# Kernel optimization log

Measured on AMD Instinct MI355X. Metric: run time of the kernel, lower is better.

Reference implementation:

```python
import jax, jax.numpy as jnp
import numpy as np

D_MODEL = 1024
D_HIDDEN = 2048
BATCH = 2
SEQ = 4096


def setup_inputs() -> dict:
    key = jax.random.key(0)
    ks = jax.random.split(key, 14)
    d, h = D_MODEL, D_HIDDEN
    s_d = 1.0 / np.sqrt(d)
    s_h = 1.0 / np.sqrt(h)
    x = jax.random.normal(ks[0], (BATCH, SEQ, d), jnp.float32)
    W1 = jax.random.normal(ks[1], (d, d), jnp.float32) * s_d
    W2 = jax.random.normal(ks[2], (d, d), jnp.float32) * s_d
    Wlast = jax.random.normal(ks[3], (d, d), jnp.float32) * s_d
    conv_w = jax.random.normal(ks[4], (d, 1, 3), jnp.float32) * 0.5  # depthwise (O, I/g=1, K)
    conv_b = jnp.zeros((d,), jnp.float32)
    A = jax.random.normal(ks[5], (h,), jnp.float32)
    Wb = jax.random.normal(ks[6], (h, d), jnp.float32) * s_d
    bb = jnp.zeros((h,), jnp.float32)
    Wc = jax.random.normal(ks[7], (d, h), jnp.float32) * s_h
    bc = jnp.zeros((d,), jnp.float32)
    Wd = jax.random.normal(ks[8], (d, d), jnp.float32) * s_d
    bd = jnp.zeros((d,), jnp.float32)
    # small delta so cumsum(delta*A) over SEQ steps stays O(1) (avoids exp overflow)
    Wdelta = jax.random.normal(ks[9], (h, d), jnp.float32) * 0.01
    bdelta = jnp.full((h,), -8.0, jnp.float32)
    return dict(x=x, W1=W1, conv_w=conv_w, conv_b=conv_b, A=A, Wb=Wb, bb=bb,
                Wc=Wc, bc=bc, Wd=Wd, bd=bd, Wdelta=Wdelta, bdelta=bdelta,
                W2=W2, Wlast=Wlast)


def reference(x, W1, conv_w, conv_b, A, Wb, bb, Wc, bc, Wd, bd, Wdelta, bdelta, W2, Wlast):
    # x: [B, L, d]
    x1 = x @ W1.T  # linear1 (no bias)
    # depthwise conv1d, kernel 3, pad 1, groups = d_model
    xc = jax.lax.conv_general_dilated(
        x1.transpose(0, 2, 1), conv_w,
        window_strides=(1,), padding=[(1, 1)],
        feature_group_count=D_MODEL,
        dimension_numbers=('NCH', 'OIH', 'NCH')) + conv_b[None, :, None]
    xa = jax.nn.silu(xc.transpose(0, 2, 1))  # [B, L, d]
    # SSM: delta/A/B discretization + cumprod-cumsum scan along sequence
    delta = jax.nn.softplus(xa @ Wdelta.T + bdelta)  # [B, L, h]
    A_bar = jnp.exp(delta * A)
    B_bar = delta * (xa @ Wb.T + bb)
    A_cum = jnp.cumprod(A_bar, axis=1)
    h_st = jnp.cumsum(B_bar / A_cum, axis=1) * A_cum  # [B, L, h]
    out_ssm = (h_st @ Wc.T + bc) + (xa @ Wd.T + bd)  # [B, L, d]
    # gated residual
    x_res = jax.nn.silu(out_ssm @ W2.T)
    z = out_ssm * x_res
    return out_ssm + z @ Wlast.T
```

## Files before the change

kernel.cpp:

```cpp
#include <hip/hip_runtime.h>
#include <cstdint>
#include <cstddef>

#define DMODEL 1024
#define DH 2048
#define BATCH 2
#define SEQ 4096
#define MROWS (BATCH*SEQ)
#define CHUNK 64
#define NCHUNK (SEQ/CHUNK)

typedef unsigned short u16;
typedef __attribute__((ext_vector_type(8))) short bf16x8;
typedef __attribute__((ext_vector_type(4))) float f32x4;

__device__ __forceinline__ u16 f2bf(float f) {
    union { float f; unsigned u; } v; v.f = f;
    unsigned r = v.u + 0x7FFFu + ((v.u >> 16) & 1u);
    return (u16)(r >> 16);
}
__device__ __forceinline__ float bf2f(u16 h) {
    union { unsigned u; float f; } v; v.u = ((unsigned)h) << 16; return v.f;
}

__device__ __forceinline__ float softplus_fast(float x) {
    if (x < -4.f) return __expf(x);
    return (x > 0.f) ? (x + log1pf(__expf(-x))) : log1pf(__expf(x));
}
__device__ __forceinline__ float silu_fast(float v) {
    return v * __fdividef(1.f, 1.f + __expf(-v));
}

__global__ void cvt_bf16(const float* __restrict__ src, u16* __restrict__ dst, int n4) {
    int i = blockIdx.x * blockDim.x + threadIdx.x;
    if (i >= n4) return;
    const float4 v = reinterpret_cast<const float4*>(src)[i];
    ushort4 o;
    o.x = f2bf(v.x); o.y = f2bf(v.y); o.z = f2bf(v.z); o.w = f2bf(v.w);
    reinterpret_cast<ushort4*>(dst)[i] = o;
}

__device__ __forceinline__ void gload_lds16(const void* g, void* l) {
    __builtin_amdgcn_global_load_lds(
        (const __attribute__((address_space(1))) void*)g,
        (__attribute__((address_space(3))) void*)l,
        16, 0, 0);
}

template<int EP, bool TWOK>
__global__ __launch_bounds__(256, 4) void gemm_bt(
    const u16* __restrict__ A1, const u16* __restrict__ B1, int K1,
    const u16* __restrict__ A2, const u16* __restrict__ B2, int K2,
    float* __restrict__ C, u16* __restrict__ Cb, u16* __restrict__ Cb2,
    const float* __restrict__ bias, const float* __restrict__ bias2,
    const float* __restrict__ aux,
    int M, int N)
{
    __shared__ __align__(16) char smem[32768];
    u16* As = (u16*)smem;
    u16* Bs = (u16*)(smem + 16384);
    float* ep = (float*)smem;

    const int tid = threadIdx.x;

    const int nwg = gridDim.x * gridDim.y;
    int wg = blockIdx.y * gridDim.x + blockIdx.x;
    wg = (wg & 7) * (nwg >> 3) + (wg >> 3);
    const int stile = wg >> 6;
    const int t64   = wg & 63;
    const int nSn   = gridDim.x >> 3;
    const int sm = (nSn > 0) ? stile / nSn : stile;
    const int sn = (nSn > 0) ? stile - sm * nSn : 0;
    const int m0 = (sm * 8 + (t64 >> 3)) * 128;
    const int n0 = (sn * 8 + (t64 & 7)) * 128;

    const int wave = tid >> 6, lane = tid & 63;
    const int wr = (wave >> 1) * 64;
    const int wc = (wave & 1) * 64;
    const int fr = lane & 15, fq = lane >> 4;

    f32x4 acc[4][4];
    #pragma unroll
    for (int m = 0; m < 4; m++)
        #pragma unroll
        for (int n = 0; n < 4; n++) acc[m][n] = f32x4{0.f, 0.f, 0.f, 0.f};

    const int nt1 = K1 >> 6;
    const int nt  = TWOK ? nt1 + (K2 >> 6) : nt1;

    for (int t = 0; t < nt; ++t) {
        const u16* A = A1; const u16* B = B1; int K = K1; int k0 = t << 6;
        if (TWOK && t >= nt1) { A = A2; B = B2; K = K2; k0 = (t - nt1) << 6; }
        #pragma unroll
        for (int i = 0; i < 4; ++i) {
            const int g = i*256 + tid;
            const int r = g >> 3;
            const int ch = (g & 7) ^ (r & 7);
            gload_lds16(A + (size_t)(m0 + r)*K + (k0 + ch*8), (char*)As + (size_t)g*16);
            gload_lds16(B + (size_t)(n0 + r)*K + (k0 + ch*8), (char*)Bs + (size_t)g*16);
        }
        __syncthreads();

        #pragma unroll
        for (int kk = 0; kk < 2; ++kk) {
            bf16x8 af[4], bfr[4];
            #pragma unroll
            for (int m = 0; m < 4; m++) {
                const int r = wr + m*16 + fr;
                af[m] = *reinterpret_cast<const bf16x8*>(
                    (const char*)As + r*128 + (((kk*4 + fq) ^ (r & 7)) * 16));
            }
            #pragma unroll
            for (int n = 0; n < 4; n++) {
                const int r = wc + n*16 + fr;
                bfr[n] = *reinterpret_cast<const bf16x8*>(
                    (const char*)Bs + r*128 + (((kk*4 + fq) ^ (r & 7)) * 16));
            }
            #pragma unroll
            for (int m = 0; m < 4; m++)
                #pragma unroll
                for (int n = 0; n < 4; n++)
                    acc[m][n] = __builtin_amdgcn_mfma_f32_16x16x32_bf16(af[m], bfr[n], acc[m][n], 0, 0, 0);
        }
        __syncthreads();
    }

    const bool isDelta = (EP == 4) ? (n0 < DH) : false;
    #pragma unroll
    for (int c = 0; c < 4; ++c) {
        if ((wave >> 1) == (c >> 1)) {
            const int mb = (c & 1) * 2;
            #pragma unroll
            for (int mi = 0; mi < 2; mi++) {
                #pragma unroll
                for (int n = 0; n < 4; n++) {
                    const int col = wc + n*16 + fr;
                    #pragma unroll
                    for (int j = 0; j < 4; j++)
                        ep[(mi*16 + fq*4 + j)*132 + col] = acc[mb + mi][n][j];
                }
            }
        }
        __syncthreads();
        #pragma unroll
        for (int p = 0; p < 4; ++p) {
            const int idx = p*256 + tid;
            const int row = idx >> 5, c4 = idx & 31;
            float4 v = *reinterpret_cast<const float4*>(&ep[row*132 + c4*4]);
            const int rg   = m0 + c*32 + row;
            const int colg = n0 + c4*4;
            if constexpr (EP == 4) {
                const int cc = isDelta ? colg : (colg - DH);
                const float4 bv = *reinterpret_cast<const float4*>(
                    (isDelta ? bias : bias2) + cc);
                ushort4 o;
                if (isDelta) {
                    o.x = f2bf(softplus_fast(v.x + bv.x));
                    o.y = f2bf(softplus_fast(v.y + bv.y));
                    o.z = f2bf(softplus_fast(v.z + bv.z));
                    o.w = f2bf(softplus_fast(v.w + bv.w));
                } else {
                    o.x = f2bf(v.x + bv.x); o.y = f2bf(v.y + bv.y);
                    o.z = f2bf(v.z + bv.z); o.w = f2bf(v.w + bv.w);
                }
                *reinterpret_cast<ushort4*>((isDelta ? Cb : Cb2) + (size_t)rg*DH + cc) = o;
            } else {
                if (bias) {
                    const float4 b1 = *reinterpret_cast<const float4*>(bias + colg);
                    v.x += b1.x; v.y += b1.y; v.z += b1.z; v.w += b1.w;
                }
                if (bias2) {
                    const float4 b2 = *reinterpret_cast<const float4*>(bias2 + colg);
                    v.x += b2.x; v.y += b2.y; v.z += b2.z; v.w += b2.w;
                }
                const size_t gidx = (size_t)rg * N + colg;
                if constexpr (EP == 0) {
                    ushort4 o = { f2bf(v.x), f2bf(v.y), f2bf(v.z), f2bf(v.w) };
                    *reinterpret_cast<ushort4*>(Cb + gidx) = o;
                } else if constexpr (EP == 1) {
                    *reinterpret_cast<float4*>(C + gidx) = v;
                    ushort4 o = { f2bf(v.x), f2bf(v.y), f2bf(v.z), f2bf(v.w) };
                    *reinterpret_cast<ushort4*>(Cb + gidx) = o;
                } else if constexpr (EP == 2) {
                    const float4 a = *reinterpret_cast<const float4*>(aux + gidx);
                    ushort4 o = { f2bf(a.x * silu_fast(v.x)), f2bf(a.y * silu_fast(v.y)),
                                  f2bf(a.z * silu_fast(v.z)), f2bf(a.w * silu_fast(v.w)) };
                    *reinterpret_cast<ushort4*>(Cb + gidx) = o;
                } else {
                    const float4 a = *reinterpret_cast<const float4*>(aux + gidx);
                    float4 o = { a.x + v.x, a.y + v.y, a.z + v.z, a.w + v.w };
                    *reinterpret_cast<float4*>(C + gidx) = o;
                }
            }
        }
        __syncthreads();
    }
}

__global__ void conv_silu8(const u16* __restrict__ x1, const float* __restrict__ cw,
                           const float* __restrict__ cb, u16* __restrict__ xab) {
    int t = blockIdx.x * blockDim.x + threadIdx.x;
    int c8  = t & (DMODEL/8 - 1);
    int row = t >> 7;
    int l = row & (SEQ - 1);
    const int c0 = c8 * 8;
    const size_t i0 = (size_t)row * DMODEL + c0;
    bf16x8 v0 = *reinterpret_cast<const bf16x8*>(x1 + i0);
    bf16x8 vm = {}; if (l > 0)       vm = *reinterpret_cast<const bf16x8*>(x1 + i0 - DMODEL);
    bf16x8 vp = {}; if (l < SEQ - 1) vp = *reinterpret_cast<const bf16x8*>(x1 + i0 + DMODEL);
    if (l == 0)       vm = bf16x8{};
    if (l == SEQ - 1) vp = bf16x8{};
    bf16x8 o;
    #pragma unroll
    for (int j = 0; j < 8; ++j) {
        const int c = c0 + j;
        float v = cw[c*3+0]*bf2f((u16)vm[j]) + cw[c*3+1]*bf2f((u16)v0[j])
                + cw[c*3+2]*bf2f((u16)vp[j]) + cb[c];
        o[j] = (short)f2bf(silu_fast(v));
    }
    *reinterpret_cast<bf16x8*>(xab + i0) = o;
}

__global__ void scan_chunks(const u16* __restrict__ delta, const u16* __restrict__ pBv,
                            const float* __restrict__ Avec,
                            float* __restrict__ cA, float* __restrict__ cB) {
    const int c = blockIdx.x * blockDim.x + threadIdx.x;
    const int q = blockIdx.y;
    const int b = blockIdx.z;
    const float Ac = Avec[c];
    float hA = 1.f, hB = 0.f;
    size_t base = ((size_t)b*SEQ + q*CHUNK)*DH + c;
    for (int j = 0; j < CHUNK; ++j) {
        float d = bf2f(delta[base]);
        float Abar = __expf(d * Ac);
        hA *= Abar;
        hB = Abar*hB + d * bf2f(pBv[base]);
        base += DH;
    }
    size_t o = ((size_t)b*NCHUNK + q)*DH + c;
    cA[o] = hA; cB[o] = hB;
}

__global__ void scan_prefix(const float* __restrict__ cA, const float* __restrict__ cB,
                            float* __restrict__ cH) {
    const int t = blockIdx.x * blockDim.x + threadIdx.x;
    const int b = t >> 11;
    const int c = t & (DH - 1);
    float h = 0.f;
    size_t o = ((size_t)b*NCHUNK)*DH + c;
    float a = cA[o], bb = cB[o];
    for (int q = 0; q < NCHUNK; ++q) {
        const size_t on = o + DH;
        float a2 = 0.f, b2 = 0.f;
        if (q + 1 < NCHUNK) { a2 = cA[on]; b2 = cB[on]; }
        cH[o] = h;
        h = a*h + bb;
        a = a2; bb = b2; o = on;
    }
}

__global__ void scan_apply(const u16* __restrict__ delta, const u16* __restrict__ pBv,
                           const float* __restrict__ Avec, const float* __restrict__ cH,
                           u16* __restrict__ hstb) {
    const int c = blockIdx.x * blockDim.x + threadIdx.x;
    const int q = blockIdx.y;
    const int b = blockIdx.z;
    const float Ac = Avec[c];
    float h = cH[((size_t)b*NCHUNK + q)*DH + c];
    size_t base = ((size_t)b*SEQ + q*CHUNK)*DH + c;
    for (int j = 0; j < CHUNK; ++j) {
        float d = bf2f(delta[base]);
        float Abar = __expf(d * Ac);
        h = Abar*h + d * bf2f(pBv[base]);
        hstb[base] = f2bf(h);
        base += DH;
    }
}

extern "C" void kernel_launch(void* const* d_in, const int* in_sizes, int n_in,
                              void* d_out, int out_size, void* d_ws, size_t ws_size,
                              hipStream_t stream) {
    const float* x      = (const float*)d_in[0];
    const float* W1     = (const float*)d_in[1];
    const float* conv_w = (const float*)d_in[2];
    const float* conv_b = (const float*)d_in[3];
    const float* Avec   = (const float*)d_in[4];
    const float* Wb     = (const float*)d_in[5];
    const float* bb     = (const float*)d_in[6];
    const float* Wc     = (const float*)d_in[7];
    const float* bc     = (const float*)d_in[8];
    const float* Wd     = (const float*)d_in[9];
    const float* bd     = (const float*)d_in[10];
    const float* Wdelta = (const float*)d_in[11];
    const float* bdelta = (const float*)d_in[12];
    const float* W2     = (const float*)d_in[13];
    const float* Wlast  = (const float*)d_in[14];
    float* out = (float*)d_out;
    (void)in_sizes; (void)n_in; (void)out_size;

    struct Ptrs {
        u16 *sW;
        float *cA, *cB, *cH;
        u16 *xb, *x1b, *xab, *delta, *pBv, *ossb, *hstb, *zb;
        float *oss;
        size_t total;
    };
    auto layout = [&](int passes) -> Ptrs {
        Ptrs P{};
        const size_t Mp = MROWS / passes;
        const int nb = BATCH / passes;
        size_t off = 0;
        auto al = [&](size_t bytes) -> char* {
            char* p = (char*)d_ws + off; off += (bytes + 255) & ~(size_t)255; return p;
        };
        P.sW  = (u16*)al((size_t)2*DH*DMODEL*2);
        P.cA  = (float*)al((size_t)nb*NCHUNK*DH*4);
        P.cB  = (float*)al((size_t)nb*NCHUNK*DH*4);
        P.cH  = (float*)al((size_t)nb*NCHUNK*DH*4);
        char* RA = al(Mp*DMODEL*2);
        char* RB = al(Mp*DMODEL*2);
        char* RC = al(Mp*DMODEL*2);
        char* RD = al(Mp*DH*2);
        char* RE = al(Mp*DH*2);
        char* RF = al(Mp*DH*2);
        P.xb    = (u16*)RA; P.ossb = (u16*)RA;
        P.x1b   = (u16*)RB; P.zb   = (u16*)RB;
        P.xab   = (u16*)RC;
        P.delta = (u16*)RD; P.oss  = (float*)RD;
        P.pBv   = (u16*)RE;
        P.hstb  = (u16*)RF;
        P.total = off;
        return P;
    };

    int passes = (ws_size >= layout(1).total) ? 1 : 2;
    Ptrs P = layout(passes);
    if (ws_size < P.total) return;
    const int Mp = MROWS / passes;
    const int nb = BATCH / passes;

    const dim3 blk(256);
    auto cvt = [&](const float* s, u16* d, size_t n) {
        int n4 = (int)(n / 4);
        cvt_bf16<<<dim3((n4 + 255)/256), blk, 0, stream>>>(s, d, n4);
    };
    const dim3 gD (DMODEL/128, Mp/128);
    const dim3 gDB(2*DH/128,   Mp/128);
    u16* sW2 = P.sW + (size_t)DH*DMODEL;

    for (int p = 0; p < passes; ++p) {
        const float* x_p  = x  + (size_t)p*Mp*DMODEL;
        float*      out_p = out + (size_t)p*Mp*DMODEL;

        cvt(x_p, P.xb, (size_t)Mp*DMODEL);
        cvt(W1, P.sW, (size_t)DMODEL*DMODEL);
        gemm_bt<0,false><<<gD, blk, 0, stream>>>(P.xb, P.sW, DMODEL, nullptr, nullptr, 0,
                                                 nullptr, P.x1b, nullptr, nullptr, nullptr, nullptr, Mp, DMODEL);
        conv_silu8<<<dim3(Mp*DMODEL/8/256), blk, 0, stream>>>(P.x1b, conv_w, conv_b, P.xab);
        cvt(Wdelta, P.sW, (size_t)DH*DMODEL);
        cvt(Wb,     sW2,  (size_t)DH*DMODEL);
        gemm_bt<4,false><<<gDB, blk, 0, stream>>>(P.xab, P.sW, DMODEL, nullptr, nullptr, 0,
                                                  nullptr, P.delta, P.pBv, bdelta, bb, nullptr, Mp, 2*DH);
        scan_chunks<<<dim3(DH/256, NCHUNK, nb), blk, 0, stream>>>(P.delta, P.pBv, Avec, P.cA, P.cB);
        scan_prefix<<<dim3(nb*DH/256), blk, 0, stream>>>(P.cA, P.cB, P.cH);
        scan_apply <<<dim3(DH/256, NCHUNK, nb), blk, 0, stream>>>(P.delta, P.pBv, Avec, P.cH, P.hstb);
        cvt(Wd, P.sW, (size_t)DMODEL*DMODEL);
        cvt(Wc, sW2,  (size_t)DMODEL*DH);
        gemm_bt<1,true><<<gD, blk, 0, stream>>>(P.xab, P.sW, DMODEL, P.hstb, sW2, DH,
                                                P.oss, P.ossb, nullptr, bd, bc, nullptr, Mp, DMODEL);
        cvt(W2, P.sW, (size_t)DMODEL*DMODEL);
        gemm_bt<2,false><<<gD, blk, 0, stream>>>(P.ossb, P.sW, DMODEL, nullptr, nullptr, 0,
                                                 nullptr, P.zb, nullptr, nullptr, nullptr, P.oss, Mp, DMODEL);
        cvt(Wlast, P.sW, (size_t)DMODEL*DMODEL);
        gemm_bt<3,false><<<gD, blk, 0, stream>>>(P.zb, P.sW, DMODEL, nullptr, nullptr, 0,
                                                 out_p, nullptr, nullptr, nullptr, nullptr, P.oss, Mp, DMODEL);
    }
}
```

Measured before the change: 307.2 us.

## Use 256x256-tile pipelined MFMA GEMM for delta/B projection

Adds a new GEMM kernel with 256x256 output tiles, 512 threads, a double-buffered 128KB LDS pipeline fed by direct global-to-LDS loads with XOR swizzling, and a workgroup remap that groups tiles per XCD. It is used for the fused Wdelta/Wb projection, the largest GEMM. Larger tiles raise arithmetic intensity and cut global traffic. The cost is low occupancy (one workgroup per CU) and higher register pressure from the 8x4 accumulator fragments.

```diff
diff --git a/kernel.cpp b/kernel.cpp
--- a/kernel.cpp
+++ b/kernel.cpp
@@ -45,6 +45,160 @@
         (const __attribute__((address_space(1))) void*)g,
         (__attribute__((address_space(3))) void*)l,
         16, 0, 0);
+}
+
+template<int EP>
+__global__ __launch_bounds__(512, 2) void gemm8p(
+    const u16* __restrict__ A, const u16* __restrict__ Bm, int K,
+    u16* __restrict__ Cb, u16* __restrict__ Cb2,
+    const float* __restrict__ bias, const float* __restrict__ bias2,
+    int M, int N)
+{
+    __shared__ __align__(16) char smem[131072];
+    const int tid = threadIdx.x;
+
+    const int nwg = gridDim.x * gridDim.y;
+    int wg = blockIdx.y * gridDim.x + blockIdx.x;
+    wg = (wg & 7) * (nwg >> 3) + (wg >> 3);
+    const int stile = wg >> 6;
+    const int t64   = wg & 63;
+    const int nSn   = gridDim.x >> 3;
+    const int sm = (nSn > 0) ? stile / nSn : stile;
+    const int sn = (nSn > 0) ? stile - sm * nSn : 0;
+    const int m0 = (sm * 8 + (t64 >> 3)) * 256;
+    const int n0 = (sn * 8 + (t64 & 7)) * 256;
+
+    const int wave = tid >> 6, lane = tid & 63;
+    const int gm16 = (wave >> 2) * 16;
+    const int gn   = wave & 3;
+    const int fr = lane & 15, fq = lane >> 4;
+    const int fx = fr & 7;
+
+    f32x4 acc[8][4];
+    #pragma unroll
+    for (int m = 0; m < 8; m++)
+        #pragma unroll
+        for (int n = 0; n < 4; n++) acc[m][n] = f32x4{0.f, 0.f, 0.f, 0.f};
+
+    const int nt = K >> 6;
+
+    auto stage_half = [&](int t, int isB, int h) {
+        const u16* src = isB ? Bm : A;
+        const int base0 = (isB ? n0 : m0) + h * 128;
+        char* dst = smem + (size_t)(((t & 1) * 65536) + isB * 32768 + h * 16384);
+        #pragma unroll
+        for (int j = 0; j < 2; ++j) {
+            const int g = j*512 + tid;
+            const int r = g >> 3;
+            const int ch = (g & 7) ^ (r & 7);
+            gload_lds16(src + (size_t)(base0 + r)*K + (t*64 + ch*8), dst + (size_t)g*16);
+        }
+    };
+
+    stage_half(0,1,0); stage_half(0,1,1); stage_half(0,0,0); stage_half(0,0,1);
+    stage_half(1,1,0); stage_half(1,1,1); stage_half(1,0,0);
+    asm volatile("s_waitcnt vmcnt(6)" ::: "memory");
+    __builtin_amdgcn_s_barrier();
+    __builtin_amdgcn_sched_barrier(0);
+
+    for (int t = 0; t < nt; ++t) {
+        const char* Abase = smem + (t & 1) * 65536;
+        const char* Bbase = Abase + 32768;
+        bf16x8 bfr[4][2];
+        #pragma unroll
+        for (int q = 0; q < 4; ++q) {
+            bf16x8 af[2][2];
+            #pragma unroll
+            for (int i = 0; i < 2; ++i) {
+                const int m = 2*q + i;
+                const int rl = (m & 3)*32 + gm16 + fr;
+                #pragma unroll
+                for (int kk = 0; kk < 2; ++kk)
+                    af[i][kk] = *reinterpret_cast<const bf16x8*>(
+                        Abase + (m >> 2)*16384 + rl*128 + (((kk*4 + fq) ^ fx) * 16));
+            }
+            if (q == 0) {
+                #pragma unroll
+                for (int n = 0; n < 4; ++n) {
+                    const int cl = (gn & 1)*64 + n*16 + fr;
+                    #pragma unroll
+                    for (int kk = 0; kk < 2; ++kk)
+                        bfr[n][kk] = *reinterpret_cast<const bf16x8*>(
+                            Bbase + (gn >> 1)*16384 + cl*128 + (((kk*4 + fq) ^ fx) * 16));
+                }
+            }
+            if (q == 0) { if (t + 1 < nt) stage_half(t + 1, 0, 1); }
+            else if (t + 2 < nt) {
+                if (q == 1)      stage_half(t + 2, 1, 0);
+                else if (q == 2) stage_half(t + 2, 1, 1);
+                else             stage_half(t + 2, 0, 0);
+            }
+            __builtin_amdgcn_s_barrier();
+            asm volatile("s_waitcnt lgkmcnt(0)" ::: "memory");
+            __builtin_amdgcn_sched_barrier(0);
+            __builtin_amdgcn_s_setprio(1);
+            #pragma unroll
+            for (int i = 0; i < 2; ++i)
+                #pragma unroll
+                for (int n = 0; n < 4; ++n)
+                    #pragma unroll
+                    for (int kk = 0; kk < 2; ++kk)
+                        acc[2*q + i][n] = __builtin_amdgcn_mfma_f32_16x16x32_bf16(
+                            af[i][kk], bfr[n][kk], acc[2*q + i][n], 0, 0, 0);
+            __builtin_amdgcn_s_setprio(0);
+            if (q == 3) {
+                if (t + 2 < nt) { asm volatile("s_waitcnt vmcnt(6)" ::: "memory"); }
+                else            { asm volatile("s_waitcnt vmcnt(0)" ::: "memory"); }
+            }
+            __builtin_amdgcn_s_barrier();
+            __builtin_amdgcn_sched_barrier(0);
+        }
+    }
+
+    float* ep = (float*)smem;
+    const bool isDelta = (EP == 4) ? (n0 < DH) : false;
+    #pragma unroll
+    for (int c = 0; c < 8; ++c) {
+        #pragma unroll
+        for (int n = 0; n < 4; ++n) {
+            const int col = gn*64 + n*16 + fr;
+            #pragma unroll
+            for (int j = 0; j < 4; ++j)
+                ep[(gm16 + fq*4 + j)*260 + col] = acc[c][n][j];
+        }
+        __syncthreads();
+        #pragma unroll
+        for (int p = 0; p < 4; ++p) {
+            const int idx = p*512 + tid;
+            const int row = idx >> 6, c4 = idx & 63;
+            float4 v = *reinterpret_cast<const float4*>(&ep[row*260 + c4*4]);
+            const int rg   = m0 + c*32 + row;
+            const int colg = n0 + c4*4;
+            if constexpr (EP == 4) {
+                const int cc = isDelta ? colg : (colg - DH);
+                const float4 bv = *reinterpret_cast<const float4*>(
+                    (isDelta ? bias : bias2) + cc);
+                ushort4 o;
+                if (isDelta) {
+                    o.x = f2bf(softplus_fast(v.x + bv.x));
+                    o.y = f2bf(softplus_fast(v.y + bv.y));
+                    o.z = f2bf(softplus_fast(v.z + bv.z));
+                    o.w = f2bf(softplus_fast(v.w + bv.w));
+                } else {
+                    o.x = f2bf(v.x + bv.x); o.y = f2bf(v.y + bv.y);
+                    o.z = f2bf(v.z + bv.z); o.w = f2bf(v.w + bv.w);
+                }
+                *reinterpret_cast<ushort4*>((isDelta ? Cb : Cb2) + (size_t)rg*DH + cc) = o;
+            } else {
+                float4 b1 = {0,0,0,0};
+                if (bias) b1 = *reinterpret_cast<const float4*>(bias + colg);
+                ushort4 o = { f2bf(v.x + b1.x), f2bf(v.y + b1.y),
+                              f2bf(v.z + b1.z), f2bf(v.w + b1.w) };
+                *reinterpret_cast<ushort4*>(Cb + (size_t)rg*N + colg) = o;
+            }
+        }
+        __syncthreads();
+    }
 }
 
 template<int EP, bool TWOK>
@@ -344,8 +498,8 @@
         int n4 = (int)(n / 4);
         cvt_bf16<<<dim3((n4 + 255)/256), blk, 0, stream>>>(s, d, n4);
     };
-    const dim3 gD (DMODEL/128, Mp/128);
-    const dim3 gDB(2*DH/128,   Mp/128);
+    const dim3 gD  (DMODEL/128, Mp/128);
+    const dim3 gDB8(2*DH/256,   Mp/256);
     u16* sW2 = P.sW + (size_t)DH*DMODEL;
 
     for (int p = 0; p < passes; ++p) {
@@ -359,8 +513,8 @@
         conv_silu8<<<dim3(Mp*DMODEL/8/256), blk, 0, stream>>>(P.x1b, conv_w, conv_b, P.xab);
         cvt(Wdelta, P.sW, (size_t)DH*DMODEL);
         cvt(Wb,     sW2,  (size_t)DH*DMODEL);
-        gemm_bt<4,false><<<gDB, blk, 0, stream>>>(P.xab, P.sW, DMODEL, nullptr, nullptr, 0,
-                                                  nullptr, P.delta, P.pBv, bdelta, bb, nullptr, Mp, 2*DH);
+        gemm8p<4><<<gDB8, dim3(512), 0, stream>>>(P.xab, P.sW, DMODEL,
+                                                  P.delta, P.pBv, bdelta, bb, Mp, 2*DH);
         scan_chunks<<<dim3(DH/256, NCHUNK, nb), blk, 0, stream>>>(P.delta, P.pBv, Avec, P.cA, P.cB);
         scan_prefix<<<dim3(nb*DH/256), blk, 0, stream>>>(P.cA, P.cB, P.cH);
         scan_apply <<<dim3(DH/256, NCHUNK, nb), blk, 0, stream>>>(P.delta, P.pBv, Avec, P.cH, P.hstb);
```

Measured after the change: 339.7 us. 1.11x slower.
